# Optimization experiments

Measured on AMD Instinct MI355X. Metric: run time of the kernel, lower is better.

## Reference

```python
import jax, jax.numpy as jnp
import numpy as np

D_MODEL = 1024
NUM_HEADS = 16
D_K = D_MODEL // NUM_HEADS
THETA = 10000.0
NEG_INF = -1e9


def _rope(x, positions):
    # x: [B, H, S, d_k]; rotate interleaved (even, odd) pairs as complex mult
    half = D_K // 2
    inv_freq = 1.0 / (THETA ** (jnp.arange(0, D_K, 2, dtype=jnp.float32) / D_K))  # [half]
    angles = positions.astype(jnp.float32)[:, None] * inv_freq  # [S, half]
    cos, sin = jnp.cos(angles), jnp.sin(angles)
    xe = x[..., 0::2]
    xo = x[..., 1::2]
    re = xe * cos - xo * sin
    ro = xe * sin + xo * cos
    return jnp.stack([re, ro], axis=-1).reshape(x.shape).astype(x.dtype)


def setup_inputs() -> dict:
    key = jax.random.key(0)
    ks = jax.random.split(key, 5)
    sigma = np.sqrt(2.0 / (D_MODEL + D_MODEL))
    x = jax.random.normal(ks[0], (2, 2048, D_MODEL), dtype=jnp.float32)
    mk = lambda k: (sigma * jax.random.normal(k, (D_MODEL, D_MODEL))).astype(jnp.float32)
    return {
        "x": x,
        "Wq": mk(ks[1]), "bq": jnp.zeros((D_MODEL,), jnp.float32),
        "Wk": mk(ks[2]), "bk": jnp.zeros((D_MODEL,), jnp.float32),
        "Wv": mk(ks[3]), "bv": jnp.zeros((D_MODEL,), jnp.float32),
        "Wo": mk(ks[4]), "bo": jnp.zeros((D_MODEL,), jnp.float32),
        "token_positions": jnp.arange(2048, dtype=jnp.int64) if jax.config.jax_enable_x64 else jnp.arange(2048, dtype=jnp.int32),
    }


def reference(x, Wq, bq, Wk, bk, Wv, bv, Wo, bo, token_positions):
    B, S, D = x.shape
    # Linear stores weight as [in, out] and computes x @ W.T + b
    Q = x @ Wq.T + bq
    K = x @ Wk.T + bk
    V = x @ Wv.T + bv
    def split_heads(t):  # [B,S,D] -> [B,H,S,d_k]
        return t.reshape(B, S, NUM_HEADS, D_K).transpose(0, 2, 1, 3)
    Q, K, V = split_heads(Q), split_heads(K), split_heads(V)
    # the torch forward always uses arange positions (it overwrites token_positions)
    pos = jnp.arange(S)
    Q = _rope(Q, pos)
    K = _rope(K, pos)
    scale = 1.0 / jnp.sqrt(jnp.float32(D_K))
    scores = jnp.einsum("bhqd,bhkd->bhqk", Q, K) * scale
    causal = jnp.tril(jnp.ones((S, S), dtype=bool))  # allowed where key <= query
    scores = jnp.where(causal, scores, NEG_INF)
    weights = jax.nn.softmax(scores, axis=-1)
    attn = jnp.einsum("bhqk,bhkd->bhqd", weights, V)  # [B,H,S,d_k]
    concat = attn.transpose(0, 2, 1, 3).reshape(B, S, D)
    return concat @ Wo.T + bo
```

## Files before the change

### kernel.cpp

```cpp
#include <hip/hip_runtime.h>
#include <math.h>

#define D_MODEL 1024
#define NH      16
#define DK      64
#define SEQ     2048
#define BATCH   2
#define RTOT    (BATCH*SEQ)

typedef __attribute__((ext_vector_type(8))) short bf16x8;
typedef __attribute__((ext_vector_type(4))) float f32x4;

__device__ __forceinline__ float bf2f(unsigned short u) {
    union { unsigned int i; float f; } v; v.i = ((unsigned int)u) << 16; return v.f;
}
__device__ __forceinline__ unsigned short f2bf(float f) {
    union { float f; unsigned int i; } v; v.f = f;
    unsigned int r = v.i + 0x7FFFu + ((v.i >> 16) & 1u);
    return (unsigned short)(r >> 16);
}
__device__ __forceinline__ unsigned int pack2bf(float a, float b) {
    return (unsigned int)f2bf(a) | ((unsigned int)f2bf(b) << 16);
}

__device__ __forceinline__ void gload_lds16(const unsigned short* g,
                                            unsigned short* l) {
    __builtin_amdgcn_global_load_lds(
        (const __attribute__((address_space(1))) void*)g,
        (__attribute__((address_space(3))) void*)l, 16, 0, 0);
}

__device__ __forceinline__ void stage128x32(
    const unsigned short* __restrict__ src, int ldk,
    unsigned short* lds, int w, int lane)
{
    #pragma unroll
    for (int p = 0; p < 2; ++p) {
        const int ckb = (w * 2 + p) * 64;
        const int ck  = ckb + lane;
        const int row = ck >> 2;
        const int cs  = (ck & 3) ^ ((row >> 1) & 3);
        gload_lds16(src + (size_t)row * ldk + cs * 8, lds + (size_t)ckb * 8);
    }
}

__global__ __launch_bounds__(256) void prep(
    const float* __restrict__ X,  const float* __restrict__ Wq,
    const float* __restrict__ Wk, const float* __restrict__ Wv,
    const float* __restrict__ Wo,
    unsigned short* __restrict__ Xbf, unsigned short* __restrict__ Wqkvbf,
    unsigned short* __restrict__ Wobf, float2* __restrict__ rope)
{
    const int id = blockIdx.x * 256 + threadIdx.x;
    const float* src;
    unsigned short* dst;
    size_t off;
    if (id < 524288) {
        src = X; dst = Xbf; off = (size_t)id * 8;
    } else {
        const int j   = id - 524288;
        const int mat = j >> 17;
        off = (size_t)(j & 131071) * 8;
        src = (mat == 0) ? Wq : (mat == 1) ? Wk : (mat == 2) ? Wv : Wo;
        dst = (mat < 3) ? (Wqkvbf + (size_t)mat * 1048576) : Wobf;
    }
    const float4 a = *(const float4*)&src[off];
    const float4 b = *(const float4*)&src[off + 4];
    uint4 p;
    p.x = pack2bf(a.x, a.y); p.y = pack2bf(a.z, a.w);
    p.z = pack2bf(b.x, b.y); p.w = pack2bf(b.z, b.w);
    *(uint4*)&dst[off] = p;

    if (id < SEQ * 32) {
        const int s  = id >> 5;
        const int fi = id & 31;
        const float ang = (float)s * powf(10000.0f, -(float)(2 * fi) * (1.0f / 64.0f));
        float c, sn;
        sincosf(ang, &c, &sn);
        rope[id] = make_float2(c, sn);
    }
}

__global__ __launch_bounds__(256) void gemm_qkv_bf(
    const unsigned short* __restrict__ Xb, const unsigned short* __restrict__ Wall,
    const float* __restrict__ bq, const float* __restrict__ bk,
    const float* __restrict__ bv, const float2* __restrict__ rope,
    unsigned short* __restrict__ Qw, unsigned short* __restrict__ Kw,
    unsigned short* __restrict__ Vw)
{
    __shared__ unsigned short Ab[2][128 * 32];
    __shared__ unsigned short Bb[2][128 * 32];

    const int t    = threadIdx.x;
    const int ct   = blockIdx.x;
    const int mat  = ct >> 3;
    const int col0 = (ct & 7) * 128;
    const int row0 = blockIdx.y * 128;

    const unsigned short* W = Wall + (size_t)mat * 1048576;
    const float* bias = (mat == 0) ? bq : (mat == 1) ? bk : bv;
    unsigned short* Y = (mat == 0) ? Qw : (mat == 1) ? Kw : Vw;

    const int lane = t & 63;
    const int wave = t >> 6;
    const int wm   = (wave >> 1) * 64;
    const int wn   = (wave & 1) * 64;
    const int l15  = lane & 15;
    const int quad = lane >> 4;

    f32x4 acc[4][4];
    #pragma unroll
    for (int i = 0; i < 4; ++i)
        #pragma unroll
        for (int j = 0; j < 4; ++j) acc[i][j] = (f32x4){0.f, 0.f, 0.f, 0.f};

    const unsigned short* Asrc = &Xb[(size_t)row0 * D_MODEL];
    const unsigned short* Bsrc = &W[(size_t)col0 * D_MODEL];

    stage128x32(Asrc, D_MODEL, Ab[0], wave, lane);
    stage128x32(Bsrc, D_MODEL, Bb[0], wave, lane);
    __syncthreads();

    for (int kt = 0; kt < 32; ++kt) {
        const int cur = kt & 1;
        if (kt + 1 < 32) {
            stage128x32(Asrc + (kt + 1) * 32, D_MODEL, Ab[cur ^ 1], wave, lane);
            stage128x32(Bsrc + (kt + 1) * 32, D_MODEL, Bb[cur ^ 1], wave, lane);
        }
        bf16x8 af[4], bfr[4];
        #pragma unroll
        for (int i = 0; i < 4; ++i) {
            const int r = wm + i * 16 + l15;
            af[i] = *(const bf16x8*)&Ab[cur][r * 32 + ((quad ^ ((r >> 1) & 3)) * 8)];
        }
        #pragma unroll
        for (int j = 0; j < 4; ++j) {
            const int r = wn + j * 16 + l15;
            bfr[j] = *(const bf16x8*)&Bb[cur][r * 32 + ((quad ^ ((r >> 1) & 3)) * 8)];
        }
        #pragma unroll
        for (int i = 0; i < 4; ++i)
            #pragma unroll
            for (int j = 0; j < 4; ++j)
                acc[i][j] = __builtin_amdgcn_mfma_f32_16x16x32_bf16(
                    af[i], bfr[j], acc[i][j], 0, 0, 0);
        __syncthreads();
    }

    #pragma unroll
    for (int i = 0; i < 4; ++i) {
        #pragma unroll
        for (int j = 0; j < 4; ++j) {
            const int cl = col0 + wn + j * 16 + l15;
            const int h  = cl >> 6;
            const int dk = cl & 63;
            const int fi = (cl & 63) >> 1;
            const float bsv = bias[cl];
            #pragma unroll
            for (int r = 0; r < 4; ++r) {
                const int row = row0 + wm + i * 16 + quad * 4 + r;
                const int s   = row & (SEQ - 1);
                const int b   = row >> 11;
                float v = acc[i][j][r] + bsv;
                if (mat < 2) {
                    const float2 cs = rope[s * 32 + fi];
                    const float p = __shfl_xor(v, 1, 64);
                    v = v * cs.x + ((l15 & 1) ? -p * cs.y : p * cs.y);
                }
                Y[((size_t)(b * NH + h) * SEQ + s) * DK + dk] = f2bf(v);
            }
        }
    }
}

__global__ __launch_bounds__(256) void gemm_qkv_f32(
    const float* __restrict__ X,
    const float* __restrict__ Wq, const float* __restrict__ bq,
    const float* __restrict__ Wk, const float* __restrict__ bk,
    const float* __restrict__ Wv, const float* __restrict__ bv,
    unsigned short* __restrict__ Qw, unsigned short* __restrict__ Kw,
    unsigned short* __restrict__ Vw)
{
    __shared__ unsigned short Ab[128 * 40];
    __shared__ unsigned short Bb[128 * 40];

    const int t    = threadIdx.x;
    const int ct   = blockIdx.x;
    const int mat  = ct >> 3;
    const int col0 = (ct & 7) * 128;
    const int row0 = blockIdx.y * 128;

    const float* W    = (mat == 0) ? Wq : (mat == 1) ? Wk : Wv;
    const float* bias = (mat == 0) ? bq : (mat == 1) ? bk : bv;
    unsigned short* Y = (mat == 0) ? Qw : (mat == 1) ? Kw : Vw;

    const int srow  = t >> 1;
    const int skseg = (t & 1) * 16;

    const int lane = t & 63;
    const int wave = t >> 6;
    const int wm   = (wave >> 1) * 64;
    const int wn   = (wave & 1) * 64;
    const int l15  = lane & 15;
    const int quad = lane >> 4;

    f32x4 acc[4][4];
    #pragma unroll
    for (int i = 0; i < 4; ++i)
        #pragma unroll
        for (int j = 0; j < 4; ++j) acc[i][j] = (f32x4){0.f, 0.f, 0.f, 0.f};

    for (int k0 = 0; k0 < D_MODEL; k0 += 32) {
        const float* xs = &X[(size_t)(row0 + srow) * D_MODEL + k0 + skseg];
        const float* ws = &W[(size_t)(col0 + srow) * D_MODEL + k0 + skseg];
        float4 x0 = *(const float4*)&xs[0],  x1 = *(const float4*)&xs[4];
        float4 x2 = *(const float4*)&xs[8],  x3 = *(const float4*)&xs[12];
        float4 w0 = *(const float4*)&ws[0],  w1 = *(const float4*)&ws[4];
        float4 w2 = *(const float4*)&ws[8],  w3 = *(const float4*)&ws[12];
        uint4 pa0, pa1, pb0, pb1;
        pa0.x = pack2bf(x0.x, x0.y); pa0.y = pack2bf(x0.z, x0.w);
        pa0.z = pack2bf(x1.x, x1.y); pa0.w = pack2bf(x1.z, x1.w);
        pa1.x = pack2bf(x2.x, x2.y); pa1.y = pack2bf(x2.z, x2.w);
        pa1.z = pack2bf(x3.x, x3.y); pa1.w = pack2bf(x3.z, x3.w);
        pb0.x = pack2bf(w0.x, w0.y); pb0.y = pack2bf(w0.z, w0.w);
        pb0.z = pack2bf(w1.x, w1.y); pb0.w = pack2bf(w1.z, w1.w);
        pb1.x = pack2bf(w2.x, w2.y); pb1.y = pack2bf(w2.z, w2.w);
        pb1.z = pack2bf(w3.x, w3.y); pb1.w = pack2bf(w3.z, w3.w);
        __syncthreads();
        *(uint4*)&Ab[srow * 40 + skseg]     = pa0;
        *(uint4*)&Ab[srow * 40 + skseg + 8] = pa1;
        *(uint4*)&Bb[srow * 40 + skseg]     = pb0;
        *(uint4*)&Bb[srow * 40 + skseg + 8] = pb1;
        __syncthreads();

        bf16x8 af[4], bfr[4];
        #pragma unroll
        for (int i = 0; i < 4; ++i)
            af[i] = *(const bf16x8*)&Ab[(wm + i * 16 + l15) * 40 + quad * 8];
        #pragma unroll
        for (int j = 0; j < 4; ++j)
            bfr[j] = *(const bf16x8*)&Bb[(wn + j * 16 + l15) * 40 + quad * 8];
        #pragma unroll
        for (int i = 0; i < 4; ++i)
            #pragma unroll
            for (int j = 0; j < 4; ++j)
                acc[i][j] = __builtin_amdgcn_mfma_f32_16x16x32_bf16(
                    af[i], bfr[j], acc[i][j], 0, 0, 0);
    }

    float invj[4];
    #pragma unroll
    for (int j = 0; j < 4; ++j) {
        const int cl = col0 + wn + j * 16 + l15;
        const int fi = (cl & 63) >> 1;
        invj[j] = powf(10000.0f, -(float)(2 * fi) * (1.0f / 64.0f));
    }
    #pragma unroll
    for (int i = 0; i < 4; ++i) {
        #pragma unroll
        for (int j = 0; j < 4; ++j) {
            const int cl = col0 + wn + j * 16 + l15;
            const int h  = cl >> 6;
            const int dk = cl & 63;
            const float bsv = bias[cl];
            #pragma unroll
            for (int r = 0; r < 4; ++r) {
                const int row = row0 + wm + i * 16 + quad * 4 + r;
                const int s   = row & (SEQ - 1);
                const int b   = row >> 11;
                float v = acc[i][j][r] + bsv;
                if (mat < 2) {
                    float c, sn;
                    sincosf((float)s * invj[j], &c, &sn);
                    const float p = __shfl_xor(v, 1, 64);
                    v = v * c + ((l15 & 1) ? -p * sn : p * sn);
                }
                Y[((size_t)(b * NH + h) * SEQ + s) * DK + dk] = f2bf(v);
            }
        }
    }
}

__global__ __launch_bounds__(256) void gemm_out_bf(
    const unsigned short* __restrict__ A, const unsigned short* __restrict__ W,
    const float* __restrict__ bias, float* __restrict__ out)
{
    __shared__ unsigned short Ab[2][128 * 32];
    __shared__ unsigned short Bb[2][128 * 32];

    const int t    = threadIdx.x;
    const int col0 = blockIdx.x * 128;
    const int row0 = blockIdx.y * 128;

    const int lane = t & 63;
    const int wave = t >> 6;
    const int wm   = (wave >> 1) * 64;
    const int wn   = (wave & 1) * 64;
    const int l15  = lane & 15;
    const int quad = lane >> 4;

    f32x4 acc[4][4];
    #pragma unroll
    for (int i = 0; i < 4; ++i)
        #pragma unroll
        for (int j = 0; j < 4; ++j) acc[i][j] = (f32x4){0.f, 0.f, 0.f, 0.f};

    const unsigned short* Asrc = &A[(size_t)row0 * D_MODEL];
    const unsigned short* Bsrc = &W[(size_t)col0 * D_MODEL];

    stage128x32(Asrc, D_MODEL, Ab[0], wave, lane);
    stage128x32(Bsrc, D_MODEL, Bb[0], wave, lane);
    __syncthreads();

    for (int kt = 0; kt < 32; ++kt) {
        const int cur = kt & 1;
        if (kt + 1 < 32) {
            stage128x32(Asrc + (kt + 1) * 32, D_MODEL, Ab[cur ^ 1], wave, lane);
            stage128x32(Bsrc + (kt + 1) * 32, D_MODEL, Bb[cur ^ 1], wave, lane);
        }
        bf16x8 af[4], bfr[4];
        #pragma unroll
        for (int i = 0; i < 4; ++i) {
            const int r = wm + i * 16 + l15;
            af[i] = *(const bf16x8*)&Ab[cur][r * 32 + ((quad ^ ((r >> 1) & 3)) * 8)];
        }
        #pragma unroll
        for (int j = 0; j < 4; ++j) {
            const int r = wn + j * 16 + l15;
            bfr[j] = *(const bf16x8*)&Bb[cur][r * 32 + ((quad ^ ((r >> 1) & 3)) * 8)];
        }
        #pragma unroll
        for (int i = 0; i < 4; ++i)
            #pragma unroll
            for (int j = 0; j < 4; ++j)
                acc[i][j] = __builtin_amdgcn_mfma_f32_16x16x32_bf16(
                    af[i], bfr[j], acc[i][j], 0, 0, 0);
        __syncthreads();
    }

    #pragma unroll
    for (int i = 0; i < 4; ++i) {
        #pragma unroll
        for (int j = 0; j < 4; ++j) {
            const int col = col0 + wn + j * 16 + l15;
            const float bsv = bias[col];
            #pragma unroll
            for (int r = 0; r < 4; ++r) {
                const int row = row0 + wm + i * 16 + quad * 4 + r;
                out[(size_t)row * D_MODEL + col] = acc[i][j][r] + bsv;
            }
        }
    }
}

__global__ __launch_bounds__(256) void gemm_out_f32(
    const unsigned short* __restrict__ A, const float* __restrict__ W,
    const float* __restrict__ bias, float* __restrict__ out)
{
    __shared__ unsigned short Ab[128 * 40];
    __shared__ unsigned short Bb[128 * 40];

    const int t    = threadIdx.x;
    const int col0 = blockIdx.x * 128;
    const int row0 = blockIdx.y * 128;

    const int srow  = t >> 1;
    const int skseg = (t & 1) * 16;

    const int lane = t & 63;
    const int wave = t >> 6;
    const int wm   = (wave >> 1) * 64;
    const int wn   = (wave & 1) * 64;
    const int l15  = lane & 15;
    const int quad = lane >> 4;

    f32x4 acc[4][4];
    #pragma unroll
    for (int i = 0; i < 4; ++i)
        #pragma unroll
        for (int j = 0; j < 4; ++j) acc[i][j] = (f32x4){0.f, 0.f, 0.f, 0.f};

    for (int k0 = 0; k0 < D_MODEL; k0 += 32) {
        const unsigned short* as = &A[(size_t)(row0 + srow) * D_MODEL + k0 + skseg];
        uint4 ua0 = *(const uint4*)&as[0];
        uint4 ua1 = *(const uint4*)&as[8];
        const float* ws = &W[(size_t)(col0 + srow) * D_MODEL + k0 + skseg];
        float4 w0 = *(const float4*)&ws[0],  w1 = *(const float4*)&ws[4];
        float4 w2 = *(const float4*)&ws[8],  w3 = *(const float4*)&ws[12];
        uint4 pb0, pb1;
        pb0.x = pack2bf(w0.x, w0.y); pb0.y = pack2bf(w0.z, w0.w);
        pb0.z = pack2bf(w1.x, w1.y); pb0.w = pack2bf(w1.z, w1.w);
        pb1.x = pack2bf(w2.x, w2.y); pb1.y = pack2bf(w2.z, w2.w);
        pb1.z = pack2bf(w3.x, w3.y); pb1.w = pack2bf(w3.z, w3.w);
        __syncthreads();
        *(uint4*)&Ab[srow * 40 + skseg]     = ua0;
        *(uint4*)&Ab[srow * 40 + skseg + 8] = ua1;
        *(uint4*)&Bb[srow * 40 + skseg]     = pb0;
        *(uint4*)&Bb[srow * 40 + skseg + 8] = pb1;
        __syncthreads();

        bf16x8 af[4], bfr[4];
        #pragma unroll
        for (int i = 0; i < 4; ++i)
            af[i] = *(const bf16x8*)&Ab[(wm + i * 16 + l15) * 40 + quad * 8];
        #pragma unroll
        for (int j = 0; j < 4; ++j)
            bfr[j] = *(const bf16x8*)&Bb[(wn + j * 16 + l15) * 40 + quad * 8];
        #pragma unroll
        for (int i = 0; i < 4; ++i)
            #pragma unroll
            for (int j = 0; j < 4; ++j)
                acc[i][j] = __builtin_amdgcn_mfma_f32_16x16x32_bf16(
                    af[i], bfr[j], acc[i][j], 0, 0, 0);
    }

    #pragma unroll
    for (int i = 0; i < 4; ++i) {
        #pragma unroll
        for (int j = 0; j < 4; ++j) {
            const int col = col0 + wn + j * 16 + l15;
            const float bsv = bias[col];
            #pragma unroll
            for (int r = 0; r < 4; ++r) {
                const int row = row0 + wm + i * 16 + quad * 4 + r;
                out[(size_t)row * D_MODEL + col] = acc[i][j][r] + bsv;
            }
        }
    }
}

#define DEFER_THR 16.0f

__device__ __forceinline__ void attn_tile_proc(
    const f32x4* sc, const bf16x8* vf, unsigned short* Psw,
    float* m, float* lsum, f32x4* od,
    bool diag, int w, int l15, int quad)
{
    float s[4][4];
    float pmax[4];
    #pragma unroll
    for (int r = 0; r < 4; ++r) pmax[r] = -3.0e38f;
    #pragma unroll
    for (int kc = 0; kc < 4; ++kc) {
        const int kcol = kc * 16 + l15;
        #pragma unroll
        for (int r = 0; r < 4; ++r) {
            float v = sc[kc][r] * 0.125f;
            if (diag) {
                const int qr = w * 16 + quad * 4 + r;
                if (kcol > qr) v = -1.0e9f;
            }
            s[kc][r] = v;
            pmax[r] = fmaxf(pmax[r], v);
        }
    }

    bool ok = true;
    #pragma unroll
    for (int r = 0; r < 4; ++r) ok = ok && (pmax[r] <= m[r] + DEFER_THR);
    if (!__all(ok)) {
        #pragma unroll
        for (int r = 0; r < 4; ++r) {
            float rmax = pmax[r];
            #pragma unroll
            for (int mk = 1; mk < 16; mk <<= 1)
                rmax = fmaxf(rmax, __shfl_xor(rmax, mk, 64));
            const float mnew  = fmaxf(m[r], rmax);
            const float alpha = __expf(m[r] - mnew);
            m[r] = mnew;
            lsum[r] *= alpha;
            #pragma unroll
            for (int dt = 0; dt < 4; ++dt) od[dt][r] *= alpha;
        }
    }

    #pragma unroll
    for (int r = 0; r < 4; ++r) {
        #pragma unroll
        for (int kc = 0; kc < 4; ++kc) {
            const float pv = __expf(s[kc][r] - m[r]);
            Psw[(quad * 4 + r) * 72 + kc * 16 + l15] = f2bf(pv);
        }
    }

    asm volatile("s_waitcnt lgkmcnt(0)" ::: "memory");

    bf16x8 pa0 = *(const bf16x8*)&Psw[l15 * 72 + quad * 8];
    bf16x8 pa1 = *(const bf16x8*)&Psw[l15 * 72 + 32 + quad * 8];

    bf16x8 ones;
    #pragma unroll
    for (int e = 0; e < 8; ++e) ones[e] = (short)0x3F80;

    __builtin_amdgcn_s_setprio(1);
    f32x4 rs = (f32x4){0.f, 0.f, 0.f, 0.f};
    rs = __builtin_amdgcn_mfma_f32_16x16x32_bf16(pa0, ones, rs, 0, 0, 0);
    rs = __builtin_amdgcn_mfma_f32_16x16x32_bf16(pa1, ones, rs, 0, 0, 0);
    #pragma unroll
    for (int dt = 0; dt < 4; ++dt) {
        od[dt] = __builtin_amdgcn_mfma_f32_16x16x32_bf16(pa0, vf[dt * 2],     od[dt], 0, 0, 0);
        od[dt] = __builtin_amdgcn_mfma_f32_16x16x32_bf16(pa1, vf[dt * 2 + 1], od[dt], 0, 0, 0);
    }
    __builtin_amdgcn_s_setprio(0);

    #pragma unroll
    for (int r = 0; r < 4; ++r) lsum[r] += rs[r];
}

__global__ __launch_bounds__(256) void attn_kernel(
    const unsigned short* __restrict__ Q, const unsigned short* __restrict__ K,
    const unsigned short* __restrict__ V, unsigned short* __restrict__ Out)
{
    __shared__ unsigned short Ks[64 * 72];
    __shared__ unsigned short Vt[64 * 72];
    __shared__ unsigned short Ps[4][16 * 72];

    const int qtA = blockIdx.x;
    const int qtB = (SEQ / 64 - 1) - qtA;
    const int bh  = blockIdx.y;
    const unsigned short* Qb = Q + (size_t)bh * SEQ * DK;
    const unsigned short* Kb = K + (size_t)bh * SEQ * DK;
    const unsigned short* Vb = V + (size_t)bh * SEQ * DK;

    const int t    = threadIdx.x;
    const int lane = t & 63;
    const int w    = t >> 6;
    const int l15  = lane & 15;
    const int quad = lane >> 4;

    const int qrowA = qtA * 64 + w * 16 + l15;
    const int qrowB = qtB * 64 + w * 16 + l15;
    bf16x8 qa0 = *(const bf16x8*)&Qb[(size_t)qrowA * DK + quad * 8];
    bf16x8 qa1 = *(const bf16x8*)&Qb[(size_t)qrowA * DK + 32 + quad * 8];
    bf16x8 qb0 = *(const bf16x8*)&Qb[(size_t)qrowB * DK + quad * 8];
    bf16x8 qb1 = *(const bf16x8*)&Qb[(size_t)qrowB * DK + 32 + quad * 8];

    f32x4 odA[4], odB[4];
    float mA[4], lsA[4], mB[4], lsB[4];
    #pragma unroll
    for (int r = 0; r < 4; ++r) {
        odA[r] = (f32x4){0.f, 0.f, 0.f, 0.f};
        odB[r] = (f32x4){0.f, 0.f, 0.f, 0.f};
        mA[r] = -3.0e38f; lsA[r] = 0.0f;
        mB[r] = -3.0e38f; lsB[r] = 0.0f;
    }

    const int tk = t >> 3;
    const int tc = t & 7;

    bf16x8 kv0 = *(const bf16x8*)&Kb[((size_t)tk) * DK + tc * 8];
    bf16x8 kv1 = *(const bf16x8*)&Kb[((size_t)(32 + tk)) * DK + tc * 8];
    bf16x8 vv0 = *(const bf16x8*)&Vb[((size_t)tk) * DK + tc * 8];
    bf16x8 vv1 = *(const bf16x8*)&Vb[((size_t)(32 + tk)) * DK + tc * 8];

    const int kp0 = tk ^ (tc * 8);
    const int kp1 = (32 + tk) ^ (tc * 8);

    for (int j = 0; j <= qtB; ++j) {
        __syncthreads();
        *(bf16x8*)&Ks[tk * 72 + tc * 8]        = kv0;
        *(bf16x8*)&Ks[(32 + tk) * 72 + tc * 8] = kv1;
        #pragma unroll
        for (int e = 0; e < 8; ++e) {
            Vt[(tc * 8 + e) * 72 + kp0] = (unsigned short)vv0[e];
            Vt[(tc * 8 + e) * 72 + kp1] = (unsigned short)vv1[e];
        }
        __syncthreads();

        if (j < qtB) {
            const size_t nb = (size_t)((j + 1) * 64);
            kv0 = *(const bf16x8*)&Kb[(nb + tk) * DK + tc * 8];
            kv1 = *(const bf16x8*)&Kb[(nb + 32 + tk) * DK + tc * 8];
            vv0 = *(const bf16x8*)&Vb[(nb + tk) * DK + tc * 8];
            vv1 = *(const bf16x8*)&Vb[(nb + 32 + tk) * DK + tc * 8];
        }

        const bool doA = (j <= qtA);

        bf16x8 kf[8];
        #pragma unroll
        for (int kc = 0; kc < 4; ++kc) {
            kf[kc * 2]     = *(const bf16x8*)&Ks[(kc * 16 + l15) * 72 + quad * 8];
            kf[kc * 2 + 1] = *(const bf16x8*)&Ks[(kc * 16 + l15) * 72 + 32 + quad * 8];
        }

        f32x4 scA[4], scB[4];
        __builtin_amdgcn_s_setprio(1);
        #pragma unroll
        for (int kc = 0; kc < 4; ++kc) {
            f32x4 z = (f32x4){0.f, 0.f, 0.f, 0.f};
            z = __builtin_amdgcn_mfma_f32_16x16x32_bf16(qb0, kf[kc * 2],     z, 0, 0, 0);
            z = __builtin_amdgcn_mfma_f32_16x16x32_bf16(qb1, kf[kc * 2 + 1], z, 0, 0, 0);
            scB[kc] = z;
        }
        if (doA) {
            #pragma unroll
            for (int kc = 0; kc < 4; ++kc) {
                f32x4 z = (f32x4){0.f, 0.f, 0.f, 0.f};
                z = __builtin_amdgcn_mfma_f32_16x16x32_bf16(qa0, kf[kc * 2],     z, 0, 0, 0);
                z = __builtin_amdgcn_mfma_f32_16x16x32_bf16(qa1, kf[kc * 2 + 1], z, 0, 0, 0);
                scA[kc] = z;
            }
        }
        __builtin_amdgcn_s_setprio(0);

        bf16x8 vf[8];
        #pragma unroll
        for (int dt = 0; dt < 4; ++dt) {
            const int d  = dt * 16 + l15;
            const int sw = d & 0x38;
            vf[dt * 2]     = *(const bf16x8*)&Vt[d * 72 + ((quad * 8) ^ sw)];
            vf[dt * 2 + 1] = *(const bf16x8*)&Vt[d * 72 + ((32 + quad * 8) ^ sw)];
        }

        if (doA)
            attn_tile_proc(scA, vf, &Ps[w][0], mA, lsA, odA, (j == qtA), w, l15, quad);
        attn_tile_proc(scB, vf, &Ps[w][0], mB, lsB, odB, (j == qtB), w, l15, quad);
    }

    const int b = bh >> 4;
    const int h = bh & 15;
    #pragma unroll
    for (int r = 0; r < 4; ++r) {
        const float rlA = 1.0f / lsA[r];
        const float rlB = 1.0f / lsB[r];
        const int qA = qtA * 64 + w * 16 + quad * 4 + r;
        const int qB = qtB * 64 + w * 16 + quad * 4 + r;
        #pragma unroll
        for (int dt = 0; dt < 4; ++dt) {
            Out[((size_t)(b * SEQ + qA)) * D_MODEL + h * DK + dt * 16 + l15] =
                f2bf(odA[dt][r] * rlA);
            Out[((size_t)(b * SEQ + qB)) * D_MODEL + h * DK + dt * 16 + l15] =
                f2bf(odB[dt][r] * rlB);
        }
    }
}

extern "C" void kernel_launch(void* const* d_in, const int* in_sizes, int n_in,
                              void* d_out, int out_size, void* d_ws, size_t ws_size,
                              hipStream_t stream) {
    const float* x  = (const float*)d_in[0];
    const float* Wq = (const float*)d_in[1];
    const float* bq = (const float*)d_in[2];
    const float* Wk = (const float*)d_in[3];
    const float* bk = (const float*)d_in[4];
    const float* Wv = (const float*)d_in[5];
    const float* bv = (const float*)d_in[6];
    const float* Wo = (const float*)d_in[7];
    const float* bo = (const float*)d_in[8];

    const size_t E = (size_t)RTOT * D_MODEL;
    float* out = (float*)d_out;
    dim3 blk(256);

    const size_t WS_NEED = (4 * E + 4 * (size_t)D_MODEL * D_MODEL) * 2
                         + (size_t)SEQ * 32 * sizeof(float2);

    unsigned short* Qws = (unsigned short*)d_ws;
    unsigned short* Kws = Qws + E;
    unsigned short* Vws = Kws + E;
    unsigned short* AXs = Vws + E;

    if (ws_size >= WS_NEED) {
        unsigned short* Wqkv = AXs + E;
        unsigned short* Wobf = Wqkv + (size_t)3 * D_MODEL * D_MODEL;
        float2*         rope = (float2*)(Wobf + (size_t)D_MODEL * D_MODEL);

        prep<<<4096, blk, 0, stream>>>(x, Wq, Wk, Wv, Wo, AXs, Wqkv, Wobf, rope);

        dim3 gq(24, RTOT / 128);
        gemm_qkv_bf<<<gq, blk, 0, stream>>>(AXs, Wqkv, bq, bk, bv, rope,
                                            Qws, Kws, Vws);

        dim3 ga(SEQ / 128, BATCH * NH);
        attn_kernel<<<ga, blk, 0, stream>>>(Qws, Kws, Vws, AXs);

        dim3 go(D_MODEL / 128, RTOT / 128);
        gemm_out_bf<<<go, blk, 0, stream>>>(AXs, Wobf, bo, out);
    } else {
        dim3 gq(24, RTOT / 128);
        gemm_qkv_f32<<<gq, blk, 0, stream>>>(x, Wq, bq, Wk, bk, Wv, bv,
                                             Qws, Kws, Vws);

        dim3 ga(SEQ / 128, BATCH * NH);
        attn_kernel<<<ga, blk, 0, stream>>>(Qws, Kws, Vws, AXs);

        dim3 go(D_MODEL / 128, RTOT / 128);
        gemm_out_f32<<<go, blk, 0, stream>>>(AXs, Wo, bo, out);
    }
}
```

Before: 222.5 us.

## Compute transposed scores to keep P in registers, dropping LDS round-trip

```diff
diff --git a/kernel.cpp b/kernel.cpp
--- a/kernel.cpp
+++ b/kernel.cpp
@@ -432,79 +432,63 @@
 #define DEFER_THR 16.0f
 
 __device__ __forceinline__ void attn_tile_proc(
-    const f32x4* sc, const bf16x8* vf, unsigned short* Psw,
-    float* m, float* lsum, f32x4* od,
+    const f32x4* sc, const bf16x8* vf,
+    float& m, float& lsum, f32x4* od,
     bool diag, int w, int l15, int quad)
 {
     float s[4][4];
-    float pmax[4];
-    #pragma unroll
-    for (int r = 0; r < 4; ++r) pmax[r] = -3.0e38f;
+    float pmax = -3.0e38f;
     #pragma unroll
     for (int kc = 0; kc < 4; ++kc) {
-        const int kcol = kc * 16 + l15;
+        const int kbase = 8 * quad + 4 * (kc & 1) + 32 * (kc >> 1);
         #pragma unroll
         for (int r = 0; r < 4; ++r) {
             float v = sc[kc][r] * 0.125f;
-            if (diag) {
-                const int qr = w * 16 + quad * 4 + r;
-                if (kcol > qr) v = -1.0e9f;
-            }
+            if (diag && (kbase + r > w * 16 + l15)) v = -1.0e9f;
             s[kc][r] = v;
-            pmax[r] = fmaxf(pmax[r], v);
-        }
-    }
-
-    bool ok = true;
-    #pragma unroll
-    for (int r = 0; r < 4; ++r) ok = ok && (pmax[r] <= m[r] + DEFER_THR);
-    if (!__all(ok)) {
+            pmax = fmaxf(pmax, v);
+        }
+    }
+    pmax = fmaxf(pmax, __shfl_xor(pmax, 16, 64));
+    pmax = fmaxf(pmax, __shfl_xor(pmax, 32, 64));
+
+    if (!__all(pmax <= m + DEFER_THR)) {
+        const float mnew  = fmaxf(m, pmax);
+        const float alpha = __expf(m - mnew);
+        m = mnew;
+        lsum *= alpha;
         #pragma unroll
         for (int r = 0; r < 4; ++r) {
-            float rmax = pmax[r];
-            #pragma unroll
-            for (int mk = 1; mk < 16; mk <<= 1)
-                rmax = fmaxf(rmax, __shfl_xor(rmax, mk, 64));
-            const float mnew  = fmaxf(m[r], rmax);
-            const float alpha = __expf(m[r] - mnew);
-            m[r] = mnew;
-            lsum[r] *= alpha;
-            #pragma unroll
-            for (int dt = 0; dt < 4; ++dt) od[dt][r] *= alpha;
-        }
-    }
-
-    #pragma unroll
-    for (int r = 0; r < 4; ++r) {
-        #pragma unroll
-        for (int kc = 0; kc < 4; ++kc) {
-            const float pv = __expf(s[kc][r] - m[r]);
-            Psw[(quad * 4 + r) * 72 + kc * 16 + l15] = f2bf(pv);
-        }
-    }
-
-    asm volatile("s_waitcnt lgkmcnt(0)" ::: "memory");
-
-    bf16x8 pa0 = *(const bf16x8*)&Psw[l15 * 72 + quad * 8];
-    bf16x8 pa1 = *(const bf16x8*)&Psw[l15 * 72 + 32 + quad * 8];
-
-    bf16x8 ones;
-    #pragma unroll
-    for (int e = 0; e < 8; ++e) ones[e] = (short)0x3F80;
+            const float ar = __shfl(alpha, quad * 20 + r, 64);
+            #pragma unroll
+            for (int dt = 0; dt < 4; ++dt) od[dt][r] *= ar;
+        }
+    }
+
+    bf16x8 pa0, pa1;
+    float rsum = 0.0f;
+    #pragma unroll
+    for (int kc = 0; kc < 4; ++kc) {
+        #pragma unroll
+        for (int r = 0; r < 4; ++r) {
+            const unsigned short b = f2bf(__expf(s[kc][r] - m));
+            rsum += bf2f(b);
+            const int e = 4 * (kc & 1) + r;
+            if ((kc >> 1) == 0) pa0[e] = (short)b;
+            else                pa1[e] = (short)b;
+        }
+    }
+    rsum += __shfl_xor(rsum, 16, 64);
+    rsum += __shfl_xor(rsum, 32, 64);
+    lsum += rsum;
 
     __builtin_amdgcn_s_setprio(1);
-    f32x4 rs = (f32x4){0.f, 0.f, 0.f, 0.f};
-    rs = __builtin_amdgcn_mfma_f32_16x16x32_bf16(pa0, ones, rs, 0, 0, 0);
-    rs = __builtin_amdgcn_mfma_f32_16x16x32_bf16(pa1, ones, rs, 0, 0, 0);
     #pragma unroll
     for (int dt = 0; dt < 4; ++dt) {
         od[dt] = __builtin_amdgcn_mfma_f32_16x16x32_bf16(pa0, vf[dt * 2],     od[dt], 0, 0, 0);
         od[dt] = __builtin_amdgcn_mfma_f32_16x16x32_bf16(pa1, vf[dt * 2 + 1], od[dt], 0, 0, 0);
     }
     __builtin_amdgcn_s_setprio(0);
-
-    #pragma unroll
-    for (int r = 0; r < 4; ++r) lsum[r] += rs[r];
 }
 
 __global__ __launch_bounds__(256) void attn_kernel(
@@ -513,7 +497,6 @@
 {
     __shared__ unsigned short Ks[64 * 72];
     __shared__ unsigned short Vt[64 * 72];
-    __shared__ unsigned short Ps[4][16 * 72];
 
     const int qtA = blockIdx.x;
     const int qtB = (SEQ / 64 - 1) - qtA;
@@ -536,13 +519,11 @@
     bf16x8 qb1 = *(const bf16x8*)&Qb[(size_t)qrowB * DK + 32 + quad * 8];
 
     f32x4 odA[4], odB[4];
-    float mA[4], lsA[4], mB[4], lsB[4];
+    float mA = -3.0e38f, lsA = 0.0f, mB = -3.0e38f, lsB = 0.0f;
     #pragma unroll
     for (int r = 0; r < 4; ++r) {
         odA[r] = (f32x4){0.f, 0.f, 0.f, 0.f};
         odB[r] = (f32x4){0.f, 0.f, 0.f, 0.f};
-        mA[r] = -3.0e38f; lsA[r] = 0.0f;
-        mB[r] = -3.0e38f; lsB[r] = 0.0f;
     }
 
     const int tk = t >> 3;
@@ -555,11 +536,13 @@
 
     const int kp0 = tk ^ (tc * 8);
     const int kp1 = (32 + tk) ^ (tc * 8);
+    const int ksw = (tk >> 3) & 3;
+    const int kc0 = ((tc & 4) | ((tc & 3) ^ ksw)) * 8;
 
     for (int j = 0; j <= qtB; ++j) {
         __syncthreads();
-        *(bf16x8*)&Ks[tk * 72 + tc * 8]        = kv0;
-        *(bf16x8*)&Ks[(32 + tk) * 72 + tc * 8] = kv1;
+        *(bf16x8*)&Ks[tk * 72 + kc0]        = kv0;
+        *(bf16x8*)&Ks[(32 + tk) * 72 + kc0] = kv1;
         #pragma unroll
         for (int e = 0; e < 8; ++e) {
             Vt[(tc * 8 + e) * 72 + kp0] = (unsigned short)vv0[e];
@@ -580,8 +563,11 @@
         bf16x8 kf[8];
         #pragma unroll
         for (int kc = 0; kc < 4; ++kc) {
-            kf[kc * 2]     = *(const bf16x8*)&Ks[(kc * 16 + l15) * 72 + quad * 8];
-            kf[kc * 2 + 1] = *(const bf16x8*)&Ks[(kc * 16 + l15) * 72 + 32 + quad * 8];
+            const int kr = ((l15 >> 2) << 3) + ((kc & 1) << 2)
+                         + ((kc >> 1) << 5) + (l15 & 3);
+            const int cs = (quad ^ ((kr >> 3) & 3)) * 8;
+            kf[kc * 2]     = *(const bf16x8*)&Ks[kr * 72 + cs];
+            kf[kc * 2 + 1] = *(const bf16x8*)&Ks[kr * 72 + 32 + cs];
         }
 
         f32x4 scA[4], scB[4];
@@ -589,16 +575,16 @@
         #pragma unroll
         for (int kc = 0; kc < 4; ++kc) {
             f32x4 z = (f32x4){0.f, 0.f, 0.f, 0.f};
-            z = __builtin_amdgcn_mfma_f32_16x16x32_bf16(qb0, kf[kc * 2],     z, 0, 0, 0);
-            z = __builtin_amdgcn_mfma_f32_16x16x32_bf16(qb1, kf[kc * 2 + 1], z, 0, 0, 0);
+            z = __builtin_amdgcn_mfma_f32_16x16x32_bf16(kf[kc * 2],     qb0, z, 0, 0, 0);
+            z = __builtin_amdgcn_mfma_f32_16x16x32_bf16(kf[kc * 2 + 1], qb1, z, 0, 0, 0);
             scB[kc] = z;
         }
         if (doA) {
             #pragma unroll
             for (int kc = 0; kc < 4; ++kc) {
                 f32x4 z = (f32x4){0.f, 0.f, 0.f, 0.f};
-                z = __builtin_amdgcn_mfma_f32_16x16x32_bf16(qa0, kf[kc * 2],     z, 0, 0, 0);
-                z = __builtin_amdgcn_mfma_f32_16x16x32_bf16(qa1, kf[kc * 2 + 1], z, 0, 0, 0);
+                z = __builtin_amdgcn_mfma_f32_16x16x32_bf16(kf[kc * 2],     qa0, z, 0, 0, 0);
+                z = __builtin_amdgcn_mfma_f32_16x16x32_bf16(kf[kc * 2 + 1], qa1, z, 0, 0, 0);
                 scA[kc] = z;
             }
         }
@@ -614,16 +600,16 @@
         }
 
         if (doA)
-            attn_tile_proc(scA, vf, &Ps[w][0], mA, lsA, odA, (j == qtA), w, l15, quad);
-        attn_tile_proc(scB, vf, &Ps[w][0], mB, lsB, odB, (j == qtB), w, l15, quad);
+            attn_tile_proc(scA, vf, mA, lsA, odA, (j == qtA), w, l15, quad);
+        attn_tile_proc(scB, vf, mB, lsB, odB, (j == qtB), w, l15, quad);
     }
 
     const int b = bh >> 4;
     const int h = bh & 15;
     #pragma unroll
     for (int r = 0; r < 4; ++r) {
-        const float rlA = 1.0f / lsA[r];
-        const float rlB = 1.0f / lsB[r];
+        const float rlA = 1.0f / __shfl(lsA, quad * 20 + r, 64);
+        const float rlB = 1.0f / __shfl(lsB, quad * 20 + r, 64);
         const int qA = qtA * 64 + w * 16 + quad * 4 + r;
         const int qB = qtB * 64 + w * 16 + quad * 4 + r;
         #pragma unroll
```

Result: no change. 226.1 us (+1.6%).
